# Kernel tuning notes

Hardware: AMD Instinct MI355X
Metric: run time of the kernel (lower is better)

Reference implementation:

```python
import jax, jax.numpy as jnp
import numpy as np
from jax import lax

FEAT_STRIDE = 16
NMS_THRESH = 0.7
N_PRE = 6000   # test-mode n_test_pre_nms
N_POST = 300   # test-mode n_test_post_nms
MIN_SIZE = 16.0
SCALE = 1.0
RATIOS = (0.5, 1.0, 2.0)
ANCHOR_SCALES = (8, 16, 32)
BASE = 16
N_ANCHOR = len(RATIOS) * len(ANCHOR_SCALES)  # 9


def _anchor_base():
    py = px = BASE / 2.0
    ab = np.zeros((N_ANCHOR, 4), np.float32)
    for i, r in enumerate(RATIOS):
        for j, s in enumerate(ANCHOR_SCALES):
            h = BASE * s * np.sqrt(r)
            w = BASE * s * np.sqrt(1.0 / r)
            k = i * len(ANCHOR_SCALES) + j
            ab[k] = [py - h / 2.0, px - w / 2.0, py + h / 2.0, px + w / 2.0]
    return ab


def _anchors(hh, ww):
    # enumerate_shifted_anchor: (y1,x1,y2,x2) anchors for every feature cell
    ab = _anchor_base()
    sy = np.arange(0, hh * FEAT_STRIDE, FEAT_STRIDE)
    sx = np.arange(0, ww * FEAT_STRIDE, FEAT_STRIDE)
    SX, SY = np.meshgrid(sx, sy)
    shift = np.stack([SY.ravel(), SX.ravel(), SY.ravel(), SX.ravel()], 1)
    anc = (ab[None, :, :] + shift[:, None, :]).reshape(-1, 4).astype(np.float32)
    return jnp.asarray(anc)


def _iou(b):
    # b: [N,4] (y1,x1,y2,x2) -> [N,N] IoU
    y1, x1, y2, x2 = b[:, 0], b[:, 1], b[:, 2], b[:, 3]
    area = (y2 - y1) * (x2 - x1)
    ih = jnp.clip(jnp.minimum(y2[:, None], y2[None, :]) - jnp.maximum(y1[:, None], y1[None, :]), 0.0)
    iw = jnp.clip(jnp.minimum(x2[:, None], x2[None, :]) - jnp.maximum(x1[:, None], x1[None, :]), 0.0)
    inter = ih * iw
    return inter / (area[:, None] + area[None, :] - inter + 1e-9)


def _propose(loc, fg, anchor, img_h, img_w):
    # loc:[M,4] fg:[M] anchor:[M,4]  -> padded [N_POST,4] rois + valid mask
    ah = anchor[:, 2] - anchor[:, 0]
    aw = anchor[:, 3] - anchor[:, 1]
    acy = anchor[:, 0] + 0.5 * ah
    acx = anchor[:, 1] + 0.5 * aw
    cy = loc[:, 0] * ah + acy
    cx = loc[:, 1] * aw + acx
    h = jnp.exp(loc[:, 2]) * ah
    w = jnp.exp(loc[:, 3]) * aw
    roi = jnp.stack([
        jnp.clip(cy - 0.5 * h, 0.0, img_h),
        jnp.clip(cx - 0.5 * w, 0.0, img_w),
        jnp.clip(cy + 0.5 * h, 0.0, img_h),
        jnp.clip(cx + 0.5 * w, 0.0, img_w),
    ], axis=1)
    hs = roi[:, 2] - roi[:, 0]
    ws = roi[:, 3] - roi[:, 1]
    ms = MIN_SIZE * SCALE
    valid = (hs >= ms) & (ws >= ms)
    sc = jnp.where(valid, fg, -jnp.inf)  # drop too-small boxes from ranking
    top_sc, idx = lax.top_k(sc, N_PRE)   # score-sorted pre-NMS candidates
    boxes = roi[idx]
    ok = lax.stop_gradient(jnp.isfinite(top_sc))
    sup = lax.stop_gradient(_iou(boxes) > NMS_THRESH)  # [N_PRE,N_PRE]
    tri = jnp.arange(N_PRE)

    def body(i, keep):
        suppressed = jnp.any(keep & sup[:, i] & (tri < i))
        return keep.at[i].set(ok[i] & ~suppressed)

    keep = lax.fori_loop(0, N_PRE, body, jnp.zeros((N_PRE,), bool))
    rank = jnp.cumsum(keep.astype(jnp.int32)) - 1
    sel = keep & (rank < N_POST)
    tgt = jnp.where(sel, rank, N_POST)  # N_POST is out-of-bounds -> dropped
    out = jnp.zeros((N_POST, 4), boxes.dtype).at[tgt].set(boxes, mode='drop')
    vmask = jnp.zeros((N_POST,), bool).at[tgt].set(True, mode='drop')
    return out, vmask


def reference(x, conv1_w, conv1_b, score_w, score_b, loc_w, loc_b, img_h, img_w):
    n, _, hh, ww = x.shape
    anchor = _anchors(hh, ww)
    h = jax.nn.relu(
        lax.conv_general_dilated(x, conv1_w, (1, 1), 'SAME',
                                 dimension_numbers=('NCHW', 'OIHW', 'NCHW'))
        + conv1_b[None, :, None, None])
    locs = jnp.einsum('nchw,oc->nohw', h, loc_w[:, :, 0, 0]) + loc_b[None, :, None, None]
    scr = jnp.einsum('nchw,oc->nohw', h, score_w[:, :, 0, 0]) + score_b[None, :, None, None]
    rpn_locs = locs.transpose(0, 2, 3, 1).reshape(n, -1, 4)          # [n,M,4]
    scr_t = scr.transpose(0, 2, 3, 1)                                 # [n,hh,ww,2A]
    soft = jax.nn.softmax(scr_t.reshape(n, hh, ww, N_ANCHOR, 2), axis=-1)
    fg = soft[..., 1].reshape(n, -1)                                  # [n,M]
    rpn_scores = scr_t.reshape(n, -1, 2)
    rois, vmask = jax.vmap(lambda l, f: _propose(l, f, anchor, img_h, img_w))(rpn_locs, fg)
    roi_indices = jnp.broadcast_to(jnp.arange(n, dtype=jnp.int32)[:, None], (n, N_POST))
    return rpn_locs, rpn_scores, rois, roi_indices, anchor, vmask


def setup_inputs() -> dict:
    key = jax.random.key(0)
    ks = jax.random.split(key, 4)
    x = jax.random.normal(ks[0], (2, 512, 64, 64), jnp.float32)
    conv1_w = 0.01 * jax.random.normal(ks[1], (512, 512, 3, 3), jnp.float32)
    conv1_b = jnp.zeros((512,), jnp.float32)
    score_w = 0.01 * jax.random.normal(ks[2], (N_ANCHOR * 2, 512, 1, 1), jnp.float32)
    score_b = jnp.zeros((N_ANCHOR * 2,), jnp.float32)
    loc_w = 0.01 * jax.random.normal(ks[3], (N_ANCHOR * 4, 512, 1, 1), jnp.float32)
    loc_b = jnp.zeros((N_ANCHOR * 4,), jnp.float32)
    return {"x": x, "conv1_w": conv1_w, "conv1_b": conv1_b,
            "score_w": score_w, "score_b": score_b,
            "loc_w": loc_w, "loc_b": loc_b,
            "img_h": 1024, "img_w": 1024}
```

## Files before the change

### kernel.cpp

```cpp
#include <hip/hip_runtime.h>
#include <hip/hip_bf16.h>
#include <math.h>
#include <cstdint>

typedef unsigned long long u64;
typedef unsigned int u32;
typedef _Float16 half8 __attribute__((ext_vector_type(8)));
typedef float floatx4 __attribute__((ext_vector_type(4)));

#define NANCH 36864
#define SEG 65536
#define N_PRE 6000
#define N_POST 300
#define NW 96
#define NPADC 6144
#define CAP 8192

#define O0 0
#define O1 294912
#define O2 442368
#define O3 444768
#define O4 445368
#define O5 592824

#define WS_XHI   0
#define WS_XLO   2097152
#define WS_WHI   4194304
#define WS_WLO   5373952
#define WS_WSLT  6553600
#define WS_WSLB  6586368
#define WS_H     6586432
#define WS_GUARD 10780736
#define WS_FG    0
#define WS_ROI   73728
#define WS_KEYS  368640
#define WS_SBOX  630784
#define WS_ALIVE 679936
#define WS_CBUF  680320
#define WS_HIST  713088
#define WS_RANK  844160
#define WS_MASK  4194304

#define HSCALE 9.5367431640625e-07f

__device__ __forceinline__ void gl_lds16(const void* g, void* l) {
  __builtin_amdgcn_global_load_lds(
      (const __attribute__((address_space(1))) u32*)g,
      (__attribute__((address_space(3))) u32*)l, 16, 0, 0);
}

__device__ __forceinline__ u64 bcast64(u64 v, int src) {
  u32 lo = (u32)__shfl((int)(v & 0xFFFFFFFFull), src);
  u32 hi = (u32)__shfl((int)(v >> 32), src);
  return ((u64)hi << 32) | lo;
}

__device__ __forceinline__ int SCX(int t) { return t + (t >> 5); }

__global__ __launch_bounds__(256) void prep_all(
    const float* __restrict__ x, const float* __restrict__ w,
    const float* __restrict__ lw, const float* __restrict__ sw,
    const float* __restrict__ lb, const float* __restrict__ sb,
    float4* __restrict__ h, float4* __restrict__ guard,
    _Float16* __restrict__ xhi, _Float16* __restrict__ xlo,
    _Float16* __restrict__ whi, _Float16* __restrict__ wlo,
    float* __restrict__ wslt, float* __restrict__ wslb) {
  __shared__ float s[64 * 65];
  const int b = blockIdx.x, tid = threadIdx.x;
  if (b < 4097) {
    int idx = b * 256 + tid;
    if (idx < 1048576) h[idx] = make_float4(0.f, 0.f, 0.f, 0.f);
    else if (idx < 1048576 + 16) guard[idx - 1048576] = make_float4(0.f, 0.f, 0.f, 0.f);
    return;
  }
  if (b < 5121) {
    int l = b - 4097;
    int pt = l & 63, cg = (l >> 6) & 7, n = l >> 9;
    const int c0 = cg << 6, p0 = pt << 6;
#pragma unroll
    for (int kk = 0; kk < 16; ++kk) {
      int e = tid + (kk << 8);
      int ci = e >> 6, pi = e & 63;
      s[ci * 65 + pi] = x[(((size_t)(n * 512 + c0 + ci)) << 12) + p0 + pi];
    }
    __syncthreads();
#pragma unroll
    for (int kk = 0; kk < 16; ++kk) {
      int e = tid + (kk << 8);
      int ci = e & 63, pi = e >> 6;
      float sv = s[ci * 65 + pi] * 1024.f;
      _Float16 hi = (_Float16)sv;
      _Float16 lo = (_Float16)(sv - (float)hi);
      size_t off = (((size_t)(n << 12) + p0 + pi) << 9) + c0 + ci;
      xhi[off] = hi;
      xlo[off] = lo;
    }
    return;
  }
  if (b < 5697) {
    int l = b - 5121;
    int ct = l & 7, ot = (l >> 3) & 7, t = l >> 6;
    const int c0 = ct << 6, o0 = ot << 6;
#pragma unroll
    for (int kk = 0; kk < 16; ++kk) {
      int e = tid + (kk << 8);
      int ci = e & 63, oi = e >> 6;
      float sv = w[(size_t)(o0 + oi) * 4608 + (c0 + ci) * 9 + t] * 1024.f;
      _Float16 hi = (_Float16)sv;
      _Float16 lo = (_Float16)(sv - (float)hi);
      size_t off = ((size_t)((t << 9) + o0 + oi) << 9) + c0 + ci;
      whi[off] = hi;
      wlo[off] = lo;
    }
    return;
  }
  {
    int e = (b - 5697) * 256 + tid;
    if (e < 32768) {
      int c = e >> 6, o = e & 63;
      float v = 0.f;
      if (o < 36) v = lw[o * 512 + c];
      else if (o < 54) v = sw[(o - 36) * 512 + c];
      wslt[e] = v;
    } else if (e < 32832) {
      int o = e - 32768;
      float v = 0.f;
      if (o < 36) v = lb[o];
      else if (o < 54) v = sb[o - 36];
      wslb[o] = v;
    }
  }
}

__global__ __launch_bounds__(256) void conv_mfma(
    const _Float16* __restrict__ xhi, const _Float16* __restrict__ xlo,
    const _Float16* __restrict__ whi, const _Float16* __restrict__ wlo,
    const float* __restrict__ guard, float* __restrict__ hout) {
  __shared__ _Float16 aHi[4 * 68 * 32];
  __shared__ _Float16 aLo[4 * 68 * 32];
  __shared__ _Float16 bHi[128 * 32];
  __shared__ _Float16 bLo[128 * 32];
  const int tid = threadIdx.x;
  const int lane = tid & 63, w = tid >> 6;
  const int ptile = blockIdx.x;
  const int og = blockIdx.y;
  const int kq = blockIdx.z;
  const int n = ptile >> 5;
  const int y0 = (ptile & 31) << 1;
  const int o0 = og << 7;
  const int l15 = lane & 15, l16 = lane >> 4;
  const int ry = w >> 1;
  const int wo = (w & 1) << 6;

  floatx4 acc[4][4];
#pragma unroll
  for (int a = 0; a < 4; ++a)
#pragma unroll
    for (int b = 0; b < 4; ++b) acc[a][b] = (floatx4)0.f;

  for (int s = 0; s < 8; ++s) {
    const int c0 = (kq << 8) + (s << 5);
    __syncthreads();
    for (int i = w; i < 17; i += 4) {
      int chunk = (i << 6) + lane;
      int p = chunk >> 2, q = chunk & 3;
      int r = p / 68, xs = p - r * 68;
      int y = y0 - 1 + r, xg = xs - 1;
      bool ok = ((unsigned)y < 64u) && ((unsigned)xg < 64u);
      size_t off = (((size_t)(n << 12) + (y << 6) + xg) << 9) + c0 + (q << 3);
      const void* gh = ok ? (const void*)(xhi + off) : (const void*)guard;
      const void* gl = ok ? (const void*)(xlo + off) : (const void*)guard;
      gl_lds16(gh, (char*)aHi + (i << 10));
      gl_lds16(gl, (char*)aLo + (i << 10));
    }
    for (int tt = 0; tt < 9; ++tt) {
      if (tt > 0) __syncthreads();
      for (int i = w; i < 8; i += 4) {
        int chunk = (i << 6) + lane;
        int row = chunk >> 2, q = chunk & 3;
        size_t off = ((size_t)((tt << 9) + o0 + row) << 9) + c0 + (q << 3);
        gl_lds16((const void*)(whi + off), (char*)bHi + (i << 10));
        gl_lds16((const void*)(wlo + off), (char*)bLo + (i << 10));
      }
      __syncthreads();

      const int dy = tt / 3, dx = tt - 3 * dy;
      half8 ah[4], al[4], bh[4], bl[4];
#pragma unroll
      for (int im = 0; im < 4; ++im) {
        int xp = (im << 4) + l15;
        int p = (ry + dy) * 68 + xp + dx;
        ah[im] = *(const half8*)&aHi[(p << 5) + (l16 << 3)];
        al[im] = *(const half8*)&aLo[(p << 5) + (l16 << 3)];
      }
#pragma unroll
      for (int in = 0; in < 4; ++in) {
        int orow = wo + (in << 4) + l15;
        bh[in] = *(const half8*)&bHi[(orow << 5) + (l16 << 3)];
        bl[in] = *(const half8*)&bLo[(orow << 5) + (l16 << 3)];
      }
#pragma unroll
      for (int im = 0; im < 4; ++im)
#pragma unroll
        for (int in = 0; in < 4; ++in) {
          acc[im][in] = __builtin_amdgcn_mfma_f32_16x16x32_f16(
              ah[im], bh[in], acc[im][in], 0, 0, 0);
          acc[im][in] = __builtin_amdgcn_mfma_f32_16x16x32_f16(
              ah[im], bl[in], acc[im][in], 0, 0, 0);
          acc[im][in] = __builtin_amdgcn_mfma_f32_16x16x32_f16(
              al[im], bh[in], acc[im][in], 0, 0, 0);
        }
    }
  }

#pragma unroll
  for (int im = 0; im < 4; ++im)
#pragma unroll
    for (int in = 0; in < 4; ++in) {
      int o = o0 + wo + (in << 4) + l15;
#pragma unroll
      for (int reg = 0; reg < 4; ++reg) {
        int m_local = (ry << 6) + (im << 4) + (l16 << 2) + reg;
        size_t off = (((size_t)(n << 12) + (y0 << 6) + m_local) << 9) + o;
        atomicAdd(&hout[off], acc[im][in][reg]);
      }
    }
}

__global__ __launch_bounds__(256) void head_kernel(
    const float* __restrict__ hbuf, const float* __restrict__ cb,
    const float* __restrict__ wslt, const float* __restrict__ wslb,
    float* __restrict__ out, float* __restrict__ fgbuf,
    uint4* __restrict__ hist4) {
  const int y = blockIdx.x, n = blockIdx.y, xq = blockIdx.z;
  __shared__ float sH[16 * 17];
  __shared__ float sWt[1024];
  __shared__ float sOut[64 * 17];
  const int tid = threadIdx.x;
  const int x4 = tid & 15, og = tid >> 4;
  const int x0 = xq << 4;

  if (xq == 0) {
    int gid = ((n << 6) + y) * 256 + tid;
    hist4[gid] = make_uint4(0u, 0u, 0u, 0u);
  }

  float acc[4];
#pragma unroll
  for (int j = 0; j < 4; ++j) acc[j] = 0.f;

  const float* hb = hbuf + (((size_t)(n << 12) + (y << 6) + x0) << 9);

  for (int c0 = 0; c0 < 512; c0 += 16) {
    __syncthreads();
    {
      int cc = tid & 15, xx = tid >> 4;
      float raw = hb[((size_t)xx << 9) + c0 + cc];
      sH[cc * 17 + xx] = fmaxf(raw * HSCALE + cb[c0 + cc], 0.f);
    }
#pragma unroll
    for (int p = 0; p < 4; ++p) {
      int e = tid + (p << 8);
      int cc = e >> 6, xx = e & 63;
      sWt[e] = wslt[((c0 + cc) << 6) + xx];
    }
    __syncthreads();
#pragma unroll
    for (int cc = 0; cc < 16; ++cc) {
      float hv = sH[cc * 17 + x4];
      float4 w0 = *(const float4*)&sWt[(cc << 6) + (og << 2)];
      acc[0] = fmaf(hv, w0.x, acc[0]);
      acc[1] = fmaf(hv, w0.y, acc[1]);
      acc[2] = fmaf(hv, w0.z, acc[2]);
      acc[3] = fmaf(hv, w0.w, acc[3]);
    }
  }
  __syncthreads();
#pragma unroll
  for (int j = 0; j < 4; ++j) {
    int o = (og << 2) + j;
    sOut[o * 17 + x4] = acc[j] + wslb[o];
  }
  __syncthreads();

  const int p0 = (n << 12) + (y << 6);
  float* locs = out + O0 + (size_t)p0 * 36 + (size_t)x0 * 36;
  for (int e = tid; e < 576; e += 256) {
    int xx = e / 36, o = e - xx * 36;
    locs[e] = sOut[o * 17 + xx];
  }
  float* scrs = out + O1 + (size_t)p0 * 18 + (size_t)x0 * 18;
  for (int e = tid; e < 288; e += 256) {
    int xx = e / 18, ss = e - xx * 18;
    scrs[e] = sOut[(36 + ss) * 17 + xx];
  }
  float* fg = fgbuf + n * NANCH + ((y << 6) + x0) * 9;
  for (int e = tid; e < 144; e += 256) {
    int xx = e / 9, a = e - xx * 9;
    float s0 = sOut[(36 + 2 * a) * 17 + xx];
    float s1 = sOut[(36 + 2 * a + 1) * 17 + xx];
    fg[e] = 1.0f / (1.0f + expf(s0 - s1));
  }
}

__global__ __launch_bounds__(256) void decode_kernel(
    const float* __restrict__ out0, const float* __restrict__ fgbuf,
    float4* __restrict__ roibuf, u64* __restrict__ keys,
    float* __restrict__ anchor_out, float* __restrict__ out,
    u32* __restrict__ hist, u64* __restrict__ cbuf,
    float4* __restrict__ sbox, u64* __restrict__ alive,
    u32* __restrict__ rankbuf,
    const int* __restrict__ imgh_p, const int* __restrict__ imgw_p) {
  int gid = blockIdx.x * 256 + threadIdx.x;
  if (gid < 16384) { cbuf[gid] = ~0ull; rankbuf[gid] = 0u; }
  if (gid < 12288) sbox[gid] = make_float4(0.f, 0.f, 0.f, 0.f);
  if (gid < 192) alive[gid] = 0ull;
  if (gid < 3600) {
    if (gid < 2400) out[O2 + gid] = 0.f;
    else if (gid < 3000) out[O3 + (gid - 2400)] = (float)((gid - 2400) / 300);
    else out[O5 + (gid - 3000)] = 0.f;
  }
  int n = gid >> 16, k = gid & (SEG - 1);
  if (k >= NANCH) return;
  int a = k % 9;
  int p = k / 9;
  int py = p >> 6, px = p & 63;

  const double R[3] = {0.5, 1.0, 2.0};
  const double S[3] = {8.0, 16.0, 32.0};
  double r = R[a / 3], s = S[a - (a / 3) * 3];
  double hd = 16.0 * s * sqrt(r);
  double wd = 16.0 * s * sqrt(1.0 / r);
  float ay1 = (float)(8.0 - hd / 2.0) + (float)(py * 16);
  float ax1 = (float)(8.0 - wd / 2.0) + (float)(px * 16);
  float ay2 = (float)(8.0 + hd / 2.0) + (float)(py * 16);
  float ax2 = (float)(8.0 + wd / 2.0) + (float)(px * 16);
  if (n == 0) {
    float* ao = anchor_out + (size_t)k * 4;
    ao[0] = ay1; ao[1] = ax1; ao[2] = ay2; ao[3] = ax2;
  }
  float ahk = ay2 - ay1, awk = ax2 - ax1;
  float acy = ay1 + 0.5f * ahk, acx = ax1 + 0.5f * awk;
  const float* lp = out0 + ((size_t)(n * NANCH + k) << 2);
  float dy = lp[0], dx = lp[1], dh = lp[2], dw = lp[3];
  float cy = dy * ahk + acy;
  float cx = dx * awk + acx;
  float bh = expf(dh) * ahk;
  float bw = expf(dw) * awk;
  float img_h = (float)imgh_p[0], img_w = (float)imgw_p[0];
  float y1 = fminf(fmaxf(cy - 0.5f * bh, 0.f), img_h);
  float x1 = fminf(fmaxf(cx - 0.5f * bw, 0.f), img_w);
  float y2 = fminf(fmaxf(cy + 0.5f * bh, 0.f), img_h);
  float x2 = fminf(fmaxf(cx + 0.5f * bw, 0.f), img_w);
  bool valid = ((y2 - y1) >= 16.f) && ((x2 - x1) >= 16.f);
  float sc = valid ? fgbuf[n * NANCH + k] : -INFINITY;
  roibuf[n * NANCH + k] = make_float4(y1, x1, y2, x2);
  unsigned int b = __float_as_uint(sc);
  unsigned int m = b ^ ((b & 0x80000000u) ? 0xFFFFFFFFu : 0x80000000u);
  u32 hk = ~m;
  keys[gid] = ((u64)hk << 32) | (unsigned int)k;
  if (hk < 0xFF800000u) atomicAdd(&hist[(n << 16) + (hk >> 16)], 1u);
}

__global__ __launch_bounds__(1024) void compact_kernel(
    const u32* __restrict__ hist, const u64* __restrict__ keys,
    u64* __restrict__ cbuf) {
  __shared__ u32 sc[1064];
  __shared__ u32 sT, sCnt;
  const int n = blockIdx.x, t = threadIdx.x;

  const uint4* hp = (const uint4*)(hist + (n << 16));
  u32 s = 0;
#pragma unroll
  for (int q = 0; q < 16; ++q) {
    uint4 v = hp[t * 16 + q];
    s += v.x + v.y + v.z + v.w;
  }
  if (t == 0) { sT = 0u; sCnt = 0u; }
  sc[SCX(t)] = s;
  __syncthreads();
  for (int off = 1; off < 1024; off <<= 1) {
    u32 v = (t >= off) ? sc[SCX(t - off)] : 0u;
    __syncthreads();
    sc[SCX(t)] += v;
    __syncthreads();
  }
  u32 total = sc[SCX(1023)];
  u32 target = total < (u32)N_PRE ? total : (u32)N_PRE;
  u32 mycum = sc[SCX(t)];
  u32 prev = t ? sc[SCX(t - 1)] : 0u;
  if (total > 0 && mycum >= target && prev < target) {
    u32 base = prev;
    int b = t << 6;
    while (true) {
      base += hist[(n << 16) + b];
      if (base >= target) break;
      ++b;
    }
    sT = (u32)b;
  }
  __syncthreads();
  const u32 T = sT;
  const bool any = (total > 0);

  const u64 below = (t & 63) ? (~0ull >> (64 - (t & 63))) : 0ull;
  for (int i = t; i < NANCH; i += 1024) {
    u64 key = keys[(n << 16) + i];
    u32 hk = (u32)(key >> 32);
    bool take = any && hk < 0xFF800000u && (hk >> 16) <= T;
    u64 bal = __ballot(take);
    u32 base = 0;
    if ((t & 63) == 0 && bal) base = atomicAdd(&sCnt, (u32)__popcll(bal));
    base = (u32)__shfl((int)base, 0);
    if (take) {
      u32 slot = base + (u32)__popcll(bal & below);
      if (slot < (u32)CAP) cbuf[(n << 13) + slot] = key;
    }
  }
}

#define JTILE 1024
__global__ __launch_bounds__(256) void rank_partial(
    const u64* __restrict__ cbuf, u32* __restrict__ rankbuf) {
  __shared__ u64 lk[JTILE];
  const int n = blockIdx.z;
  const int i = blockIdx.x * 256 + threadIdx.x;
  const int j0 = blockIdx.y * JTILE;
  const u64* cb = cbuf + (n << 13);
  const u64 mykey = cb[i];
  for (int e = threadIdx.x; e < JTILE; e += 256) lk[e] = cb[j0 + e];
  __syncthreads();
  u32 r = 0;
#pragma unroll 8
  for (int j = 0; j < JTILE; ++j) r += (lk[j] < mykey) ? 1u : 0u;
  atomicAdd(&rankbuf[(n << 13) + i], r);
}

__global__ __launch_bounds__(256) void rank_scatter(
    const u64* __restrict__ cbuf, const u32* __restrict__ rankbuf,
    const float4* __restrict__ roibuf,
    float4* __restrict__ sbox, u64* __restrict__ alive) {
  const int n = blockIdx.y;
  const int i = blockIdx.x * 256 + threadIdx.x;
  u64 mykey = cbuf[(n << 13) + i];
  if (mykey == ~0ull) return;
  u32 rank = rankbuf[(n << 13) + i];
  if (rank < (u32)N_PRE) {
    u32 k = (u32)(mykey & 0xFFFFFFFFull);
    sbox[n * NPADC + rank] = roibuf[(size_t)n * NANCH + k];
    atomicOr(&alive[n * NW + (rank >> 6)], 1ull << (rank & 63));
  }
}

__global__ __launch_bounds__(256) void build_mask(
    const float4* __restrict__ sbox, u64* __restrict__ M) {
  __shared__ float4 jb[4][64];
  __shared__ float ja[4][64];
  const int tid = threadIdx.x, lane = tid & 63, wv = tid >> 6;
  const int g = blockIdx.x, q = blockIdx.y, n = blockIdx.z;
  const float4* sb = sbox + n * NPADC;
  float4 bi = sb[(g << 6) + lane];
  float ai = (bi.z - bi.x) * (bi.w - bi.y);
  u64* Mrow = M + ((size_t)(n * NPADC + (g << 6) + lane)) * NW;
#pragma unroll
  for (int it = 0; it < 6; ++it) {
    int w = q * 24 + (it << 2) + wv;
    if (w < g) continue;
    float4 bjl = sb[(w << 6) + lane];
    jb[wv][lane] = bjl;
    ja[wv][lane] = (bjl.z - bjl.x) * (bjl.w - bjl.y);
    u64 bits = 0;
#pragma unroll 8
    for (int j = 0; j < 64; ++j) {
      float4 bj = jb[wv][j];
      float aj = ja[wv][j];
      float ih = fmaxf(fminf(bi.z, bj.z) - fmaxf(bi.x, bj.x), 0.f);
      float iw = fmaxf(fminf(bi.w, bj.w) - fmaxf(bi.y, bj.y), 0.f);
      float inter = ih * iw;
      bool bit = inter / (ai + aj - inter + 1e-9f) > 0.7f;
      bits |= ((u64)bit) << j;
    }
    Mrow[w] = bits;
  }
}

__global__ __launch_bounds__(64) void nms_reduce(
    const u64* __restrict__ M, const u64* __restrict__ alive,
    const float4* __restrict__ sbox, float* __restrict__ out) {
  const int n = blockIdx.x, lane = threadIdx.x;
  float* rois = out + O2 + n * (N_POST * 4);
  float* vmask = out + O5 + n * N_POST;
  const u64* A = alive + n * NW;
  const u64* Mb = M + (size_t)n * NPADC * NW;
  const float4* sb = sbox + n * NPADC;
  u64 aw0 = A[lane];
  u64 aw1 = (lane < 32) ? A[64 + lane] : 0ull;
  u64 accA = 0, accB = 0;
  int nk = 0;
  u64 dnext = Mb[(size_t)lane * NW + 0];
  float4 bnext = sb[lane];
  const u64 below = lane ? (~0ull >> (64 - lane)) : 0ull;

  for (int c = 0; c < 94; ++c) {
    u64 dcur = dnext;
    float4 bcur = bnext;
    if (c + 1 < 94) {
      dnext = Mb[(size_t)(((c + 1) << 6) + lane) * NW + (c + 1)];
      bnext = sb[((c + 1) << 6) + lane];
    }
    u64 wacc = (c < 64) ? bcast64(accA, c) : bcast64(accB, c - 64);
    u64 aw = (c < 64) ? bcast64(aw0, c) : bcast64(aw1, c - 64);
    u64 alive_u = aw & ~wacc;
    if (alive_u == 0ull) continue;

    u64 dmask = dcur & below;
    u64 rem = alive_u, kept = 0;
    while (rem) {
      int j = __builtin_ctzll(rem);
      kept |= 1ull << j;
      u64 col = __ballot((dmask >> j) & 1);
      rem &= ~(col | (1ull << j));
    }

    int npop = __popcll(kept);
    if ((kept >> lane) & 1ull) {
      int slot = nk + __popcll(kept & below);
      if (slot < N_POST) {
        rois[slot * 4 + 0] = bcur.x; rois[slot * 4 + 1] = bcur.y;
        rois[slot * 4 + 2] = bcur.z; rois[slot * 4 + 3] = bcur.w;
        vmask[slot] = 1.0f;
      }
    }
    if (nk + npop >= N_POST) break;
    nk += npop;

    u64 kk = kept;
    while (kk) {
      int j0 = __builtin_ctzll(kk); kk &= kk - 1;
      int j1 = kk ? __builtin_ctzll(kk) : j0; kk &= kk - 1;
      int j2 = kk ? __builtin_ctzll(kk) : j0; kk &= kk - 1;
      int j3 = kk ? __builtin_ctzll(kk) : j0; kk &= kk - 1;
      int j4 = kk ? __builtin_ctzll(kk) : j0; kk &= kk - 1;
      int j5 = kk ? __builtin_ctzll(kk) : j0; kk &= kk - 1;
      int j6 = kk ? __builtin_ctzll(kk) : j0; kk &= kk - 1;
      int j7 = kk ? __builtin_ctzll(kk) : j0; kk &= kk - 1;
      const u64* r0 = Mb + (size_t)((c << 6) + j0) * NW;
      const u64* r1 = Mb + (size_t)((c << 6) + j1) * NW;
      const u64* r2 = Mb + (size_t)((c << 6) + j2) * NW;
      const u64* r3 = Mb + (size_t)((c << 6) + j3) * NW;
      const u64* r4 = Mb + (size_t)((c << 6) + j4) * NW;
      const u64* r5 = Mb + (size_t)((c << 6) + j5) * NW;
      const u64* r6 = Mb + (size_t)((c << 6) + j6) * NW;
      const u64* r7 = Mb + (size_t)((c << 6) + j7) * NW;
      u64 oA = r0[lane] | r1[lane] | r2[lane] | r3[lane]
             | r4[lane] | r5[lane] | r6[lane] | r7[lane];
      u64 oB = 0;
      if (lane < 32)
        oB = r0[64 + lane] | r1[64 + lane] | r2[64 + lane] | r3[64 + lane]
           | r4[64 + lane] | r5[64 + lane] | r6[64 + lane] | r7[64 + lane];
      accA |= oA;
      accB |= oB;
    }
  }
}

extern "C" void kernel_launch(void* const* d_in, const int* in_sizes, int n_in,
                              void* d_out, int out_size, void* d_ws, size_t ws_size,
                              hipStream_t stream) {
  const float* x        = (const float*)d_in[0];
  const float* conv1_w  = (const float*)d_in[1];
  const float* conv1_b  = (const float*)d_in[2];
  const float* score_w  = (const float*)d_in[3];
  const float* score_b  = (const float*)d_in[4];
  const float* loc_w    = (const float*)d_in[5];
  const float* loc_b    = (const float*)d_in[6];
  const int*   imgh_p   = (const int*)d_in[7];
  const int*   imgw_p   = (const int*)d_in[8];

  float* out = (float*)d_out;
  float* ws  = (float*)d_ws;

  _Float16* xhi = (_Float16*)(ws + WS_XHI);
  _Float16* xlo = (_Float16*)(ws + WS_XLO);
  _Float16* whi = (_Float16*)(ws + WS_WHI);
  _Float16* wlo = (_Float16*)(ws + WS_WLO);
  float* wslt   = ws + WS_WSLT;
  float* wslb   = ws + WS_WSLB;
  float* hbuf   = ws + WS_H;
  float* guard  = ws + WS_GUARD;
  float* fgbuf   = ws + WS_FG;
  float4* roibuf = (float4*)(ws + WS_ROI);
  u64* keys      = (u64*)(ws + WS_KEYS);
  float4* sbox   = (float4*)(ws + WS_SBOX);
  u64* alive     = (u64*)(ws + WS_ALIVE);
  u64* cbuf      = (u64*)(ws + WS_CBUF);
  u32* hist      = (u32*)(ws + WS_HIST);
  u32* rankbuf   = (u32*)(ws + WS_RANK);
  u64* maskbuf   = (u64*)(ws + WS_MASK);

  prep_all<<<5826, 256, 0, stream>>>(x, conv1_w, loc_w, score_w, loc_b, score_b,
                                     (float4*)hbuf, (float4*)guard,
                                     xhi, xlo, whi, wlo, wslt, wslb);

  conv_mfma<<<dim3(64, 4, 2), 256, 0, stream>>>(xhi, xlo, whi, wlo, guard, hbuf);

  head_kernel<<<dim3(64, 2, 4), 256, 0, stream>>>(hbuf, conv1_b, wslt, wslb, out,
                                                  fgbuf, (uint4*)hist);
  decode_kernel<<<512, 256, 0, stream>>>(out, fgbuf, roibuf, keys,
                                         out + O4, out, hist, cbuf, sbox, alive,
                                         rankbuf, imgh_p, imgw_p);

  compact_kernel<<<2, 1024, 0, stream>>>(hist, keys, cbuf);
  rank_partial<<<dim3(32, 8, 2), 256, 0, stream>>>(cbuf, rankbuf);
  rank_scatter<<<dim3(32, 2), 256, 0, stream>>>(cbuf, rankbuf, roibuf, sbox, alive);

  build_mask<<<dim3(96, 4, 2), 256, 0, stream>>>(sbox, maskbuf);
  nms_reduce<<<2, 64, 0, stream>>>(maskbuf, alive, sbox, out);
}
```

Before: 437.5 us.

## Parallelize NMS suppression-row OR across a 1024-thread block with LDS atomics

The NMS reduce kernel grows from one wave to a 1024-thread block. Wave 0 still resolves each 64-box chunk serially and writes the kept row indices to shared memory. Waves 4-15 then OR those suppression-mask rows into a shared accumulator in parallel, eight rows per thread, using LDS atomicOr. This spreads the serial gather of mask rows across more memory parallelism. The cost is two block-wide barriers per chunk, and several waves (1-3) sit idle.

```diff
diff --git a/kernel.cpp b/kernel.cpp
--- a/kernel.cpp
+++ b/kernel.cpp
@@ -484,83 +484,110 @@
   }
 }
 
-__global__ __launch_bounds__(64) void nms_reduce(
+__global__ __launch_bounds__(1024) void nms_reduce(
     const u64* __restrict__ M, const u64* __restrict__ alive,
     const float4* __restrict__ sbox, float* __restrict__ out) {
-  const int n = blockIdx.x, lane = threadIdx.x;
+  const int n = blockIdx.x, t = threadIdx.x;
+  const int lane = t & 63, wv = t >> 6;
   float* rois = out + O2 + n * (N_POST * 4);
   float* vmask = out + O5 + n * N_POST;
   const u64* A = alive + n * NW;
   const u64* Mb = M + (size_t)n * NPADC * NW;
   const float4* sb = sbox + n * NPADC;
-  u64 aw0 = A[lane];
-  u64 aw1 = (lane < 32) ? A[64 + lane] : 0ull;
-  u64 accA = 0, accB = 0;
+
+  __shared__ u64 accLds[NW];
+  __shared__ int rowsS[64];
+  __shared__ int cntS;
+  __shared__ int doneS;
+
+  if (t < NW) accLds[t] = 0ull;
+  if (t == 0) { doneS = 0; cntS = 0; }
+
+  u64 aw0 = 0, aw1 = 0;
+  u64 dnext = 0;
+  float4 bnext = make_float4(0.f, 0.f, 0.f, 0.f);
   int nk = 0;
-  u64 dnext = Mb[(size_t)lane * NW + 0];
-  float4 bnext = sb[lane];
   const u64 below = lane ? (~0ull >> (64 - lane)) : 0ull;
+  if (wv == 0) {
+    aw0 = A[lane];
+    aw1 = (lane < 32) ? A[64 + lane] : 0ull;
+    dnext = Mb[(size_t)lane * NW + 0];
+    bnext = sb[lane];
+  }
+
+  const int u = t - 256;
+  const int word = (u >= 0) ? (u % 96) : 0;
+  const int slot = (u >= 0) ? (u / 96) : 0;
+
+  __syncthreads();
 
   for (int c = 0; c < 94; ++c) {
-    u64 dcur = dnext;
-    float4 bcur = bnext;
-    if (c + 1 < 94) {
-      dnext = Mb[(size_t)(((c + 1) << 6) + lane) * NW + (c + 1)];
-      bnext = sb[((c + 1) << 6) + lane];
-    }
-    u64 wacc = (c < 64) ? bcast64(accA, c) : bcast64(accB, c - 64);
-    u64 aw = (c < 64) ? bcast64(aw0, c) : bcast64(aw1, c - 64);
-    u64 alive_u = aw & ~wacc;
-    if (alive_u == 0ull) continue;
-
-    u64 dmask = dcur & below;
-    u64 rem = alive_u, kept = 0;
-    while (rem) {
-      int j = __builtin_ctzll(rem);
-      kept |= 1ull << j;
-      u64 col = __ballot((dmask >> j) & 1);
-      rem &= ~(col | (1ull << j));
-    }
-
-    int npop = __popcll(kept);
-    if ((kept >> lane) & 1ull) {
-      int slot = nk + __popcll(kept & below);
-      if (slot < N_POST) {
-        rois[slot * 4 + 0] = bcur.x; rois[slot * 4 + 1] = bcur.y;
-        rois[slot * 4 + 2] = bcur.z; rois[slot * 4 + 3] = bcur.w;
-        vmask[slot] = 1.0f;
+    if (wv == 0) {
+      u64 dcur = dnext;
+      float4 bcur = bnext;
+      if (c + 1 < 94) {
+        dnext = Mb[(size_t)(((c + 1) << 6) + lane) * NW + (c + 1)];
+        bnext = sb[((c + 1) << 6) + lane];
       }
-    }
-    if (nk + npop >= N_POST) break;
-    nk += npop;
-
-    u64 kk = kept;
-    while (kk) {
-      int j0 = __builtin_ctzll(kk); kk &= kk - 1;
-      int j1 = kk ? __builtin_ctzll(kk) : j0; kk &= kk - 1;
-      int j2 = kk ? __builtin_ctzll(kk) : j0; kk &= kk - 1;
-      int j3 = kk ? __builtin_ctzll(kk) : j0; kk &= kk - 1;
-      int j4 = kk ? __builtin_ctzll(kk) : j0; kk &= kk - 1;
-      int j5 = kk ? __builtin_ctzll(kk) : j0; kk &= kk - 1;
-      int j6 = kk ? __builtin_ctzll(kk) : j0; kk &= kk - 1;
-      int j7 = kk ? __builtin_ctzll(kk) : j0; kk &= kk - 1;
-      const u64* r0 = Mb + (size_t)((c << 6) + j0) * NW;
-      const u64* r1 = Mb + (size_t)((c << 6) + j1) * NW;
-      const u64* r2 = Mb + (size_t)((c << 6) + j2) * NW;
-      const u64* r3 = Mb + (size_t)((c << 6) + j3) * NW;
-      const u64* r4 = Mb + (size_t)((c << 6) + j4) * NW;
-      const u64* r5 = Mb + (size_t)((c << 6) + j5) * NW;
-      const u64* r6 = Mb + (size_t)((c << 6) + j6) * NW;
-      const u64* r7 = Mb + (size_t)((c << 6) + j7) * NW;
-      u64 oA = r0[lane] | r1[lane] | r2[lane] | r3[lane]
-             | r4[lane] | r5[lane] | r6[lane] | r7[lane];
-      u64 oB = 0;
-      if (lane < 32)
-        oB = r0[64 + lane] | r1[64 + lane] | r2[64 + lane] | r3[64 + lane]
-           | r4[64 + lane] | r5[64 + lane] | r6[64 + lane] | r7[64 + lane];
-      accA |= oA;
-      accB |= oB;
-    }
+      u64 wacc = accLds[c];
+      u64 aw = (c < 64) ? bcast64(aw0, c) : bcast64(aw1, c - 64);
+      u64 alive_u = aw & ~wacc;
+      u64 kept = 0;
+      if (alive_u) {
+        u64 dmask = dcur & below;
+        u64 rem = alive_u;
+        while (rem) {
+          int j = __builtin_ctzll(rem);
+          kept |= 1ull << j;
+          u64 col = __ballot((dmask >> j) & 1);
+          rem &= ~(col | (1ull << j));
+        }
+        int npop = __popcll(kept);
+        if ((kept >> lane) & 1ull) {
+          int oslot = nk + __popcll(kept & below);
+          if (oslot < N_POST) {
+            rois[oslot * 4 + 0] = bcur.x; rois[oslot * 4 + 1] = bcur.y;
+            rois[oslot * 4 + 2] = bcur.z; rois[oslot * 4 + 3] = bcur.w;
+            vmask[oslot] = 1.0f;
+          }
+          rowsS[__popcll(kept & below)] = (c << 6) + lane;
+        }
+        if (lane == 0) {
+          cntS = npop;
+          if (nk + npop >= N_POST) doneS = 1;
+        }
+        nk += npop;
+      } else {
+        if (lane == 0) cntS = 0;
+      }
+    }
+    __syncthreads();
+    if (doneS) break;
+    const int cnt = cntS;
+    if (cnt > 0 && u >= 0) {
+      int b0 = slot << 3;
+      if (b0 < cnt) {
+        int i1 = (b0 + 1 < cnt) ? b0 + 1 : cnt - 1;
+        int i2 = (b0 + 2 < cnt) ? b0 + 2 : cnt - 1;
+        int i3 = (b0 + 3 < cnt) ? b0 + 3 : cnt - 1;
+        int i4 = (b0 + 4 < cnt) ? b0 + 4 : cnt - 1;
+        int i5 = (b0 + 5 < cnt) ? b0 + 5 : cnt - 1;
+        int i6 = (b0 + 6 < cnt) ? b0 + 6 : cnt - 1;
+        int i7 = (b0 + 7 < cnt) ? b0 + 7 : cnt - 1;
+        const u64* r0 = Mb + (size_t)rowsS[b0] * NW;
+        const u64* r1 = Mb + (size_t)rowsS[i1] * NW;
+        const u64* r2 = Mb + (size_t)rowsS[i2] * NW;
+        const u64* r3 = Mb + (size_t)rowsS[i3] * NW;
+        const u64* r4 = Mb + (size_t)rowsS[i4] * NW;
+        const u64* r5 = Mb + (size_t)rowsS[i5] * NW;
+        const u64* r6 = Mb + (size_t)rowsS[i6] * NW;
+        const u64* r7 = Mb + (size_t)rowsS[i7] * NW;
+        u64 p = r0[word] | r1[word] | r2[word] | r3[word]
+              | r4[word] | r5[word] | r6[word] | r7[word];
+        atomicOr(&accLds[word], p);
+      }
+    }
+    __syncthreads();
   }
 }
 
@@ -615,5 +642,5 @@
   rank_scatter<<<dim3(32, 2), 256, 0, stream>>>(cbuf, rankbuf, roibuf, sbox, alive);
 
   build_mask<<<dim3(96, 4, 2), 256, 0, stream>>>(sbox, maskbuf);
-  nms_reduce<<<2, 64, 0, stream>>>(maskbuf, alive, sbox, out);
-}
+  nms_reduce<<<2, 1024, 0, stream>>>(maskbuf, alive, sbox, out);
+}
```

New measurement: 425.6 us. -2.7%, faster.
